# Performance work log

Hardware: AMD Instinct MI355X
Metric: run time of the kernel (lower is better)

## Reference

```python
import jax, jax.numpy as jnp
import numpy as np

EMBED_DIM = 768
NUM_HEADS = 12
HEAD_DIM = EMBED_DIM // NUM_HEADS
SCALE = HEAD_DIM ** -0.5
B, N = 8, 1024


def setup_inputs() -> dict:
    key = jax.random.key(0)
    ks = jax.random.split(key, 5)
    return {
        "x": jax.random.normal(ks[0], (B, N, EMBED_DIM), dtype=jnp.float32),
        "qkv_w": jax.random.normal(ks[1], (3 * EMBED_DIM, EMBED_DIM), dtype=jnp.float32) * 0.02,
        "qkv_b": jax.random.normal(ks[2], (3 * EMBED_DIM,), dtype=jnp.float32) * 0.02,
        "proj_w": jax.random.normal(ks[3], (EMBED_DIM, EMBED_DIM), dtype=jnp.float32) * 0.02,
        "proj_b": jax.random.normal(ks[4], (EMBED_DIM,), dtype=jnp.float32) * 0.02,
    }


def reference(x, qkv_w, qkv_b, proj_w, proj_b):
    b, n, c = x.shape
    h, hd = NUM_HEADS, HEAD_DIM
    # QKV projection: [b,n,3c]
    qkv = jnp.einsum("bnc,dc->bnd", x, qkv_w) + qkv_b
    qkv = qkv.reshape(b, n, 3, h, hd).transpose(2, 0, 3, 1, 4)  # [3,b,h,n,hd]
    q, k, v = qkv[0], qkv[1], qkv[2]
    # scaled dot-product attention (eager path; dropout is identity in eval)
    attn = jnp.einsum("bhqd,bhkd->bhqk", q, k) * SCALE
    attn = jax.nn.softmax(attn, axis=-1)
    out = jnp.einsum("bhqk,bhkd->bhqd", attn, v)  # [b,h,n,hd]
    out = out.transpose(0, 2, 1, 3).reshape(b, n, c)
    # output projection
    return jnp.einsum("bnc,dc->bnd", out, proj_w) + proj_b
```

## Files before the change

### kernel.cpp

```cpp
#include <hip/hip_runtime.h>
#include <hip/hip_bf16.h>

typedef __attribute__((ext_vector_type(4))) float f32x4;
typedef __attribute__((ext_vector_type(16))) float f32x16;
typedef __attribute__((ext_vector_type(8))) short short8;
typedef unsigned short u16;

#define MFMA(a, b, c) __builtin_amdgcn_mfma_f32_16x16x32_bf16((a), (b), (c), 0, 0, 0)
#define MFMA32(a, b, c) __builtin_amdgcn_mfma_f32_32x32x16_bf16((a), (b), (c), 0, 0, 0)

static constexpr int EMBED = 768;
static constexpr int NH = 12;
static constexpr int HD = 64;
static constexpr int BATCH = 8;
static constexpr int SEQ = 1024;

__device__ __forceinline__ u16 f2bu(float f) {
    __hip_bfloat16 h = __float2bfloat16(f);
    u16 u; __builtin_memcpy(&u, &h, 2); return u;
}
__device__ __forceinline__ float exp2a(float x) {
    float r; asm("v_exp_f32 %0, %1" : "=v"(r) : "v"(x)); return r;
}
__device__ __forceinline__ unsigned cvt_pk_bf16(float lo, float hi) {
    unsigned r; asm("v_cvt_pk_bf16_f32 %0, %1, %2" : "=v"(r) : "v"(lo), "v"(hi)); return r;
}
__device__ __forceinline__ void swap32(unsigned& a, unsigned& b) {
    asm volatile("v_permlane32_swap_b32 %0, %1" : "+v"(a), "+v"(b));
}
__device__ __forceinline__ short8 mk8(unsigned w0, unsigned w1, unsigned w2, unsigned w3) {
    union { unsigned u[4]; short8 s; } c;
    c.u[0] = w0; c.u[1] = w1; c.u[2] = w2; c.u[3] = w3;
    return c.s;
}

__global__ void cvt_all_k(const float* __restrict__ x, const float* __restrict__ w1,
                          const float* __restrict__ w2,
                          u16* __restrict__ xb, u16* __restrict__ wb, u16* __restrict__ pw) {
    const int n1 = BATCH * SEQ * EMBED;
    const int n2 = 3 * EMBED * EMBED;
    const int n3 = EMBED * EMBED;
    int i = (blockIdx.x * blockDim.x + threadIdx.x) * 4;
    const float* src; u16* dst;
    if (i < n1)            { src = x  + i;             dst = xb + i; }
    else if (i < n1 + n2)  { src = w1 + (i - n1);      dst = wb + (i - n1); }
    else if (i < n1+n2+n3) { src = w2 + (i - n1 - n2); dst = pw + (i - n1 - n2); }
    else return;
    float4 v = *reinterpret_cast<const float4*>(src);
    ushort4 o;
    o.x = f2bu(v.x); o.y = f2bu(v.y); o.z = f2bu(v.z); o.w = f2bu(v.w);
    *reinterpret_cast<ushort4*>(dst) = o;
}

template <int EPI, int BN>
__global__ __launch_bounds__(256)
void gemm_bt_k(const u16* __restrict__ A, const u16* __restrict__ Bw,
               const float* __restrict__ bias,
               u16* __restrict__ q_out, u16* __restrict__ k_out,
               u16* __restrict__ vt_out, float* __restrict__ f_out)
{
    constexpr int BUFB = 16384 + BN * 128;
    constexpr int NCH  = 16 + BN / 8;
    constexpr int CPW  = NCH / 4;
    constexpr int WN   = BN / 2;
    constexpr int NI   = WN / 16;

    __shared__ __attribute__((aligned(16))) char smem[2 * BUFB];
    const int tid  = threadIdx.x;
    const int wave = tid >> 6, lane = tid & 63;
    const int hi   = lane >> 4, l15 = lane & 15;
    const int wr   = wave >> 1, wc = wave & 1;
    const int bm   = blockIdx.x, bn = blockIdx.y;

    f32x4 acc[4][NI] = {};

    const size_t arow0 = (size_t)bm * 128;
    const size_t brow0 = (size_t)bn * BN;

    const u16* sptr[CPW]; int dofs[CPW];
#pragma unroll
    for (int c = 0; c < CPW; ++c) {
        int ch = c * 4 + wave;
        if (ch < 16) {
            int p    = ch * 1024 + lane * 16;
            int row  = p >> 7;
            int pcol = (p & 127) ^ ((row & 7) << 4);
            sptr[c] = A + (arow0 + row) * EMBED + (pcol >> 1);
            dofs[c] = ch * 1024;
        } else {
            int p    = (ch - 16) * 1024 + lane * 16;
            int row  = p >> 7;
            int pcol = (p & 127) ^ ((row & 7) << 4);
            sptr[c] = Bw + (brow0 + row) * EMBED + (pcol >> 1);
            dofs[c] = 16384 + (ch - 16) * 1024;
        }
    }
    auto stage = [&](int buf, int kt) {
        char* base = smem + buf * BUFB;
#pragma unroll
        for (int c = 0; c < CPW; ++c)
            __builtin_amdgcn_global_load_lds(
                (const __attribute__((address_space(1))) void*)(sptr[c] + kt),
                (__attribute__((address_space(3))) void*)(base + dofs[c]), 16, 0, 0);
    };

    const int sw_l = (l15 & 7) << 4;
    int aoff[2], boff[2];
#pragma unroll
    for (int kk = 0; kk < 2; ++kk) {
        int col = (kk * 64 + hi * 16) ^ sw_l;
        aoff[kk] = (wr * 64 + l15) * 128 + col;
        boff[kk] = 16384 + (wc * WN + l15) * 128 + col;
    }

    auto comp = [&](int buf) {
        const char* base = smem + buf * BUFB;
#pragma unroll
        for (int kk = 0; kk < 2; ++kk) {
            short8 af[4], bf[NI];
#pragma unroll
            for (int mi = 0; mi < 4; ++mi)
                af[mi] = *reinterpret_cast<const short8*>(base + aoff[kk] + mi * 2048);
#pragma unroll
            for (int ni = 0; ni < NI; ++ni)
                bf[ni] = *reinterpret_cast<const short8*>(base + boff[kk] + ni * 2048);
#pragma unroll
            for (int mi = 0; mi < 4; ++mi)
#pragma unroll
                for (int ni = 0; ni < NI; ++ni)
                    acc[mi][ni] = MFMA(af[mi], bf[ni], acc[mi][ni]);
        }
    };

    auto waitvm_bar = [&]() {
        if constexpr (CPW == 10) asm volatile("s_waitcnt vmcnt(10)" ::: "memory");
        else                     asm volatile("s_waitcnt vmcnt(8)"  ::: "memory");
        __builtin_amdgcn_s_barrier();
        __builtin_amdgcn_sched_barrier(0);
    };
    auto bar2 = [&]() {
        __builtin_amdgcn_sched_barrier(0);
        __builtin_amdgcn_s_barrier();
        __builtin_amdgcn_sched_barrier(0);
    };

    stage(0, 0);
#pragma unroll
    for (int tt = 0; tt < 5; ++tt) {
        stage(1, (2 * tt + 1) * 64);
        waitvm_bar();
        comp(0);
        bar2();
        stage(0, (2 * tt + 2) * 64);
        waitvm_bar();
        comp(1);
        bar2();
    }
    stage(1, 11 * 64);
    waitvm_bar();
    comp(0);
    bar2();
    asm volatile("s_waitcnt vmcnt(0)" ::: "memory");
    __builtin_amdgcn_s_barrier();
    __builtin_amdgcn_sched_barrier(0);
    comp(1);

#pragma unroll
    for (int mi = 0; mi < 4; ++mi) {
        int crow0 = bm * 128 + wr * 64 + mi * 16 + hi * 4;
#pragma unroll
        for (int ni = 0; ni < NI; ++ni) {
            int ccol = bn * BN + wc * WN + ni * 16 + l15;
            float bv = bias[ccol];
            if constexpr (EPI == 0) {
                int which = ccol / 768;
                int rem   = ccol - which * 768;
                int hh = rem >> 6, hd = rem & 63;
                int bb = crow0 >> 10, nn0 = crow0 & 1023;
                size_t bh = (size_t)(bb * NH + hh);
                if (which == 2) {
                    uint2 pk;
                    pk.x = cvt_pk_bf16(acc[mi][ni][0] + bv, acc[mi][ni][1] + bv);
                    pk.y = cvt_pk_bf16(acc[mi][ni][2] + bv, acc[mi][ni][3] + bv);
                    *reinterpret_cast<uint2*>(&vt_out[(bh * HD + hd) * SEQ + nn0]) = pk;
                } else if (which == 0) {
#pragma unroll
                    for (int r = 0; r < 4; ++r)
                        q_out[(bh * SEQ + nn0 + r) * HD + hd] =
                            f2bu((acc[mi][ni][r] + bv) * 0.18033688f);
                } else {
#pragma unroll
                    for (int r = 0; r < 4; ++r)
                        k_out[(bh * SEQ + nn0 + r) * HD + hd] = f2bu(acc[mi][ni][r] + bv);
                }
            } else {
#pragma unroll
                for (int r = 0; r < 4; ++r)
                    f_out[(size_t)(crow0 + r) * EMBED + ccol] = acc[mi][ni][r] + bv;
            }
        }
    }
}

__global__ __launch_bounds__(256, 3)
void attn_k(const u16* __restrict__ Q, const u16* __restrict__ K,
            const u16* __restrict__ Vt, u16* __restrict__ AO)
{
    __shared__ __attribute__((aligned(16))) u16 kv[3][8192];

    const int tid = threadIdx.x;
    const int w   = tid >> 6, lane = tid & 63;
    const int h   = lane >> 5, l31 = lane & 31;
    const int f   = blockIdx.x;
    const int xcd = f & 7, i = f >> 3;
    const int bh  = xcd * 12 + (i % 12);
    const int q0w = (i / 12) * 128 + w * 32;

    const u16* Qh = Q  + (size_t)bh * SEQ * HD;
    const u16* Kh = K  + (size_t)bh * SEQ * HD;
    const u16* Vh = Vt + (size_t)bh * HD * SEQ;

    short8 qf[4];
#pragma unroll
    for (int ds = 0; ds < 4; ++ds)
        qf[ds] = *reinterpret_cast<const short8*>(
            Qh + (size_t)(q0w + l31) * HD + ds * 16 + h * 8);
    __builtin_amdgcn_sched_barrier(0);

    const u16* sptr[4]; int doff[4]; int sadv[4];
#pragma unroll
    for (int c = 0; c < 4; ++c) {
        int ch = c * 4 + w;
        int mc = ch & 7;
        int p  = mc * 1024 + lane * 16;
        int row = p >> 7;
        int colb = (p & 127) ^ ((row & 7) << 4) ^ (((row >> 3) & 3) << 5);
        if (ch < 8) { sptr[c] = Kh + (size_t)row * HD + (colb >> 1); sadv[c] = 64 * HD; doff[c] = mc * 512; }
        else        { sptr[c] = Vh + (size_t)row * SEQ + (colb >> 1); sadv[c] = 64;     doff[c] = 4096 + mc * 512; }
    }
    auto stage = [&](int buf, int t) {
#pragma unroll
        for (int c = 0; c < 4; ++c)
            __builtin_amdgcn_global_load_lds(
                (const __attribute__((address_space(1))) void*)(sptr[c] + (size_t)t * sadv[c]),
                (__attribute__((address_space(3))) void*)(&kv[buf][doff[c]]), 16, 0, 0);
    };

    stage(0, 0);
    stage(1, 1);

    const int sw_l = ((l31 & 7) << 4) ^ (((l31 >> 3) & 3) << 5);
    int koff[4];
#pragma unroll
    for (int ds = 0; ds < 4; ++ds)
        koff[ds] = l31 * 128 + ((ds * 32 + h * 16) ^ sw_l);

    union { unsigned u[4]; short8 s; } oc;
    oc.u[0] = oc.u[1] = oc.u[2] = oc.u[3] = 0x3F803F80u;
    const short8 ones8 = oc.s;

    f32x16 accO[2] = {};
    f32x16 lsum = {};

    auto tile = [&](int BC) {
        const char* base = (const char*)kv + BC * 16384;
        f32x16 st[2] = {{0}, {0}};
        __builtin_amdgcn_s_setprio(1);
#pragma unroll
        for (int mf = 0; mf < 2; ++mf)
#pragma unroll
            for (int ds = 0; ds < 4; ++ds) {
                short8 kf = *reinterpret_cast<const short8*>(base + mf * 4096 + koff[ds]);
                st[mf] = MFMA32(kf, qf[ds], st[mf]);
            }
        __builtin_amdgcn_s_setprio(0);

        unsigned pkw[2][8];
#pragma unroll
        for (int mf = 0; mf < 2; ++mf)
#pragma unroll
            for (int p = 0; p < 8; ++p) {
                float e0 = exp2a(st[mf][2 * p]);
                float e1 = exp2a(st[mf][2 * p + 1]);
                pkw[mf][p] = cvt_pk_bf16(e0, e1);
            }

        short8 pb[4];
#pragma unroll
        for (int ks = 0; ks < 4; ++ks) {
            int mf = ks >> 1, b4 = (ks & 1) * 4;
            unsigned E0 = pkw[mf][b4 + 0], E1 = pkw[mf][b4 + 1];
            unsigned D0 = pkw[mf][b4 + 2], D1 = pkw[mf][b4 + 3];
            swap32(E0, D0);
            swap32(E1, D1);
            pb[ks] = mk8(E0, E1, D0, D1);
        }

        __builtin_amdgcn_s_setprio(1);
#pragma unroll
        for (int ks = 0; ks < 4; ++ks)
            lsum = MFMA32(ones8, pb[ks], lsum);
#pragma unroll
        for (int df = 0; df < 2; ++df)
#pragma unroll
            for (int ks = 0; ks < 4; ++ks) {
                short8 vf = *reinterpret_cast<const short8*>(base + 8192 + df * 4096 + koff[ks]);
                accO[df] = MFMA32(vf, pb[ks], accO[df]);
            }
        __builtin_amdgcn_s_setprio(0);
    };

    auto one = [&](int bc, int bs, int tn, bool ds) {
        asm volatile("s_waitcnt vmcnt(4)" ::: "memory");
        __builtin_amdgcn_s_barrier();
        __builtin_amdgcn_sched_barrier(0);
        if (ds) stage(bs, tn);
        tile(bc);
        __builtin_amdgcn_sched_barrier(0);
    };

    one(0, 2, 2, true);
    one(1, 0, 3, true);
    one(2, 1, 4, true);
    for (int g = 1; g < 5; ++g) {
        one(0, 2, 3 * g + 2, true);
        one(1, 0, 3 * g + 3, 3 * g + 3 <= 15);
        one(2, 1, 3 * g + 4, 3 * g + 4 <= 15);
    }
    asm volatile("s_waitcnt vmcnt(0)" ::: "memory");
    __builtin_amdgcn_s_barrier();
    __builtin_amdgcn_sched_barrier(0);
    tile(0);

    float linv = 1.f / lsum[0];
    const int bb = bh / NH, hh = bh - bb * NH;
    size_t rowb = ((size_t)bb * SEQ + q0w + l31) * EMBED + hh * HD;
#pragma unroll
    for (int df = 0; df < 2; ++df)
#pragma unroll
        for (int g = 0; g < 4; ++g) {
            float o0 = accO[df][4 * g + 0] * linv;
            float o1 = accO[df][4 * g + 1] * linv;
            float o2 = accO[df][4 * g + 2] * linv;
            float o3 = accO[df][4 * g + 3] * linv;
            uint2 pk;
            pk.x = cvt_pk_bf16(o0, o1);
            pk.y = cvt_pk_bf16(o2, o3);
            *reinterpret_cast<uint2*>(&AO[rowb + df * 32 + 8 * g + 4 * h]) = pk;
        }
}

extern "C" void kernel_launch(void* const* d_in, const int* in_sizes, int n_in,
                              void* d_out, int out_size, void* d_ws, size_t ws_size,
                              hipStream_t stream)
{
    const float* x      = (const float*)d_in[0];
    const float* qkv_w  = (const float*)d_in[1];
    const float* qkv_b  = (const float*)d_in[2];
    const float* proj_w = (const float*)d_in[3];
    const float* proj_b = (const float*)d_in[4];
    float* out = (float*)d_out;

    char* ws = (char*)d_ws;
    u16* xb  = (u16*)(ws);
    u16* wb  = (u16*)(ws + 12582912);
    u16* pw  = (u16*)(ws + 16121856);
    u16* qb  = (u16*)(ws + 17301504);
    u16* kb  = (u16*)(ws + 29884416);
    u16* vt  = (u16*)(ws + 42467328);
    u16* ao  = (u16*)(ws + 55050240);

    cvt_all_k<<<8448, 256, 0, stream>>>(x, qkv_w, proj_w, xb, wb, pw);

    gemm_bt_k<0, 192><<<dim3(64, 12), 256, 0, stream>>>(xb, wb, qkv_b, qb, kb, vt, nullptr);
    attn_k<<<768, 256, 0, stream>>>(qb, kb, vt, ao);
    gemm_bt_k<1, 128><<<dim3(64, 6), 256, 0, stream>>>(ao, pw, proj_b, nullptr, nullptr, nullptr, out);
}
```

Baseline: 98.34 us.

## Load GEMM A operand directly into registers, stage only B through LDS

The GEMM kernel no longer stages the A tile through shared memory. Each wave loads its A fragments straight from global memory into registers, and only the B (weight) tile is double-buffered in LDS. The loop now waits on vmcnt(0) every k-step, and launch bounds request 3 blocks per CU to raise occupancy. The projection GEMM switches to BN=96 with 8 column blocks. This cuts LDS footprint and traffic but exposes global-load latency, because A loads are uncoalesced 16-byte row reads with a full drain each iteration.

```diff
diff --git a/kernel.cpp b/kernel.cpp
--- a/kernel.cpp
+++ b/kernel.cpp
@@ -53,14 +53,14 @@
 }
 
 template <int EPI, int BN>
-__global__ __launch_bounds__(256)
+__global__ __launch_bounds__(256, 3)
 void gemm_bt_k(const u16* __restrict__ A, const u16* __restrict__ Bw,
                const float* __restrict__ bias,
                u16* __restrict__ q_out, u16* __restrict__ k_out,
                u16* __restrict__ vt_out, float* __restrict__ f_out)
 {
-    constexpr int BUFB = 16384 + BN * 128;
-    constexpr int NCH  = 16 + BN / 8;
+    constexpr int BUFB = BN * 128;
+    constexpr int NCH  = BN / 8;
     constexpr int CPW  = NCH / 4;
     constexpr int WN   = BN / 2;
     constexpr int NI   = WN / 16;
@@ -80,20 +80,12 @@
     const u16* sptr[CPW]; int dofs[CPW];
 #pragma unroll
     for (int c = 0; c < CPW; ++c) {
-        int ch = c * 4 + wave;
-        if (ch < 16) {
-            int p    = ch * 1024 + lane * 16;
-            int row  = p >> 7;
-            int pcol = (p & 127) ^ ((row & 7) << 4);
-            sptr[c] = A + (arow0 + row) * EMBED + (pcol >> 1);
-            dofs[c] = ch * 1024;
-        } else {
-            int p    = (ch - 16) * 1024 + lane * 16;
-            int row  = p >> 7;
-            int pcol = (p & 127) ^ ((row & 7) << 4);
-            sptr[c] = Bw + (brow0 + row) * EMBED + (pcol >> 1);
-            dofs[c] = 16384 + (ch - 16) * 1024;
-        }
+        int ch   = c * 4 + wave;
+        int p    = ch * 1024 + lane * 16;
+        int row  = p >> 7;
+        int pcol = (p & 127) ^ ((row & 7) << 4);
+        sptr[c] = Bw + (brow0 + row) * EMBED + (pcol >> 1);
+        dofs[c] = ch * 1024;
     }
     auto stage = [&](int buf, int kt) {
         char* base = smem + buf * BUFB;
@@ -104,66 +96,47 @@
                 (__attribute__((address_space(3))) void*)(base + dofs[c]), 16, 0, 0);
     };
 
+    const u16* abase = A + (arow0 + wr * 64 + l15) * EMBED + hi * 8;
+
     const int sw_l = (l15 & 7) << 4;
-    int aoff[2], boff[2];
-#pragma unroll
-    for (int kk = 0; kk < 2; ++kk) {
-        int col = (kk * 64 + hi * 16) ^ sw_l;
-        aoff[kk] = (wr * 64 + l15) * 128 + col;
-        boff[kk] = 16384 + (wc * WN + l15) * 128 + col;
-    }
-
-    auto comp = [&](int buf) {
-        const char* base = smem + buf * BUFB;
-#pragma unroll
-        for (int kk = 0; kk < 2; ++kk) {
-            short8 af[4], bf[NI];
+    int boff[2];
+#pragma unroll
+    for (int kk = 0; kk < 2; ++kk)
+        boff[kk] = (wc * WN + l15) * 128 + ((kk * 64 + hi * 16) ^ sw_l);
+
+    stage(0, 0);
+#pragma unroll
+    for (int t = 0; t < 12; ++t) {
+        asm volatile("s_waitcnt vmcnt(0)" ::: "memory");
+        __builtin_amdgcn_s_barrier();
+        __builtin_amdgcn_sched_barrier(0);
+        short8 af[2][4];
+#pragma unroll
+        for (int kk = 0; kk < 2; ++kk)
 #pragma unroll
             for (int mi = 0; mi < 4; ++mi)
-                af[mi] = *reinterpret_cast<const short8*>(base + aoff[kk] + mi * 2048);
-#pragma unroll
-            for (int ni = 0; ni < NI; ++ni)
-                bf[ni] = *reinterpret_cast<const short8*>(base + boff[kk] + ni * 2048);
-#pragma unroll
-            for (int mi = 0; mi < 4; ++mi)
+                af[kk][mi] = *reinterpret_cast<const short8*>(
+                    abase + (size_t)mi * 16 * EMBED + t * 64 + kk * 32);
+        __builtin_amdgcn_sched_barrier(0);
+        if (t + 1 < 12) stage((t + 1) & 1, (t + 1) * 64);
+        __builtin_amdgcn_sched_barrier(0);
+        {
+            const char* base = smem + (t & 1) * BUFB;
+#pragma unroll
+            for (int kk = 0; kk < 2; ++kk) {
+                short8 bf[NI];
 #pragma unroll
                 for (int ni = 0; ni < NI; ++ni)
-                    acc[mi][ni] = MFMA(af[mi], bf[ni], acc[mi][ni]);
+                    bf[ni] = *reinterpret_cast<const short8*>(base + boff[kk] + ni * 2048);
+#pragma unroll
+                for (int mi = 0; mi < 4; ++mi)
+#pragma unroll
+                    for (int ni = 0; ni < NI; ++ni)
+                        acc[mi][ni] = MFMA(af[kk][mi], bf[ni], acc[mi][ni]);
+            }
         }
-    };
-
-    auto waitvm_bar = [&]() {
-        if constexpr (CPW == 10) asm volatile("s_waitcnt vmcnt(10)" ::: "memory");
-        else                     asm volatile("s_waitcnt vmcnt(8)"  ::: "memory");
-        __builtin_amdgcn_s_barrier();
-        __builtin_amdgcn_sched_barrier(0);
-    };
-    auto bar2 = [&]() {
-        __builtin_amdgcn_sched_barrier(0);
-        __builtin_amdgcn_s_barrier();
-        __builtin_amdgcn_sched_barrier(0);
-    };
-
-    stage(0, 0);
-#pragma unroll
-    for (int tt = 0; tt < 5; ++tt) {
-        stage(1, (2 * tt + 1) * 64);
-        waitvm_bar();
-        comp(0);
-        bar2();
-        stage(0, (2 * tt + 2) * 64);
-        waitvm_bar();
-        comp(1);
-        bar2();
-    }
-    stage(1, 11 * 64);
-    waitvm_bar();
-    comp(0);
-    bar2();
-    asm volatile("s_waitcnt vmcnt(0)" ::: "memory");
-    __builtin_amdgcn_s_barrier();
-    __builtin_amdgcn_sched_barrier(0);
-    comp(1);
+        __builtin_amdgcn_sched_barrier(0);
+    }
 
 #pragma unroll
     for (int mi = 0; mi < 4; ++mi) {
@@ -374,5 +347,5 @@
 
     gemm_bt_k<0, 192><<<dim3(64, 12), 256, 0, stream>>>(xb, wb, qkv_b, qb, kb, vt, nullptr);
     attn_k<<<768, 256, 0, stream>>>(qb, kb, vt, ao);
-    gemm_bt_k<1, 128><<<dim3(64, 6), 256, 0, stream>>>(ao, pw, proj_b, nullptr, nullptr, nullptr, out);
-}
+    gemm_bt_k<1, 96><<<dim3(64, 8), 256, 0, stream>>>(ao, pw, proj_b, nullptr, nullptr, nullptr, out);
+}
```

Measured after the change: 139.4 us. +41.8%, slower.
